# Optimization experiments

Measured on AMD Instinct MI355X. Metric: run time of the kernel, lower is better.

Reference implementation:

```python
import jax, jax.numpy as jnp
import numpy as np
from jax import lax


def _conv3x3(x, w, b):
    # x: [b,C,H,W], w: [Cout,Cin,3,3] (OIHW), same padding, stride 1
    y = lax.conv_general_dilated(
        x, w, window_strides=(1, 1), padding='SAME',
        dimension_numbers=('NCHW', 'OIHW', 'NCHW'))
    return y + b[None, :, None, None]


def setup_inputs() -> dict:
    key = jax.random.key(0)
    ks = jax.random.split(key, 8)
    b, C, H, W = 8, 256, 64, 64
    wscale = 0.02  # keep conv outputs O(1) so softmax logits are well-conditioned
    X = jax.random.normal(ks[0], (b, C, H, W), dtype=jnp.float32)
    w1 = jax.random.normal(ks[1], (C, C, 3, 3), dtype=jnp.float32) * wscale
    b1 = jax.random.normal(ks[2], (C,), dtype=jnp.float32) * 0.01
    w2 = jax.random.normal(ks[3], (C, C, 3, 3), dtype=jnp.float32) * wscale
    b2 = jax.random.normal(ks[4], (C,), dtype=jnp.float32) * 0.01
    w3 = jax.random.normal(ks[5], (C, C, 3, 3), dtype=jnp.float32) * wscale
    b3 = jax.random.normal(ks[6], (C,), dtype=jnp.float32) * 0.01
    # alpha_init=0 in the original makes the output identically zero; use a
    # small nonzero alpha so fwd/bwd are non-degenerate for correctness checks.
    alpha = jax.random.normal(ks[7], (), dtype=jnp.float32)
    return {"X": X, "w1": w1, "b1": b1, "w2": w2, "b2": b2,
            "w3": w3, "b3": b3, "alpha": alpha}


def reference(X, w1, b1, w2, b2, w3, b3, alpha):
    b, C, H, W = X.shape
    N = H * W
    A = _conv3x3(X, w1, b1).reshape(b, C, N)  # [b,C,N]
    B = _conv3x3(X, w2, b2).reshape(b, C, N)  # [b,C,N]
    D = _conv3x3(X, w3, b3).reshape(b, C, N)  # [b,C,N]
    # M = softmax(A^T B) over last dim; M: [b,N,N]
    M = jnp.einsum('bcn,bcm->bnm', A, B)
    M = jax.nn.softmax(M, axis=-1)
    # weighted_C = M @ D^T -> [b,N,C]; then to [b,C,H,W]
    out = jnp.einsum('bnm,bcm->bcn', M, D).reshape(b, C, H, W)
    return alpha * out
```

## Files before the change

### kernel.cpp

```cpp
#include <hip/hip_runtime.h>
#include <math.h>

#define BATCH 8
#define CCH   256
#define HH    64
#define WW    64
#define NN    4096

#define BNC   (BATCH * NN * CCH)
#define WELEMS (3 * 8 * 9 * 256 * 32)

typedef __bf16   bf16x8 __attribute__((ext_vector_type(8)));
typedef _Float16 f16x8  __attribute__((ext_vector_type(8)));
typedef _Float16 f16x4  __attribute__((ext_vector_type(4)));
typedef float    f32x4  __attribute__((ext_vector_type(4)));

__global__ void wtrans_kernel(const float* __restrict__ w1,
                              const float* __restrict__ w2,
                              const float* __restrict__ w3,
                              _Float16* __restrict__ Whi,
                              _Float16* __restrict__ Wlo) {
    int e = blockIdx.x * 256 + threadIdx.x;
    int t = e;
    const int ci  = t & 31;  t >>= 5;
    const int co  = t & 255; t >>= 8;
    const int tap = t % 9;   t /= 9;
    const int cc  = t & 7;   t >>= 3;
    const int conv = t;
    const float* src = (conv == 0) ? w1 : (conv == 1) ? w2 : w3;
    const float v = src[co * 2304 + (cc * 32 + ci) * 9 + tap];
    const _Float16 h = (_Float16)v;
    Whi[e] = h;
    Wlo[e] = (_Float16)(v - (float)h);
}

__global__ __launch_bounds__(256)
void xsplit_kernel(const float* __restrict__ X,
                   _Float16* __restrict__ Xhi, _Float16* __restrict__ Xlo) {
    __shared__ float T[64][65];
    const int h = blockIdx.x, c0 = blockIdx.y * 64, bb = blockIdx.z;
    const int t = threadIdx.x;
    const int row = t >> 2, q = (t & 3) * 16;
#pragma unroll
    for (int k = 0; k < 4; ++k) {
        float4 v = *(const float4*)&X[(((size_t)bb * CCH + c0 + row) * HH + h) * WW + q + k * 4];
        *(float4*)&T[row][q + k * 4] = v;
    }
    __syncthreads();
    f16x8 h0, h1, l0, l1;
#pragma unroll
    for (int j = 0; j < 8; ++j) {
        float v = T[q + j][row];
        _Float16 hh = (_Float16)v;
        h0[j] = hh; l0[j] = (_Float16)(v - (float)hh);
    }
#pragma unroll
    for (int j = 0; j < 8; ++j) {
        float v = T[q + 8 + j][row];
        _Float16 hh = (_Float16)v;
        h1[j] = hh; l1[j] = (_Float16)(v - (float)hh);
    }
    const size_t g = (((size_t)bb * HH + h) * WW + row) * CCH + c0 + q;
    *(f16x8*)(Xhi + g) = h0;  *(f16x8*)(Xhi + g + 8) = h1;
    *(f16x8*)(Xlo + g) = l0;  *(f16x8*)(Xlo + g + 8) = l1;
}

__global__ __launch_bounds__(512, 2)
void conv_mfma_kernel(const _Float16* __restrict__ Xhi, const _Float16* __restrict__ Xlo,
                      const _Float16* __restrict__ Whi, const _Float16* __restrict__ Wlo,
                      const float* __restrict__ b1, const float* __restrict__ b2,
                      const float* __restrict__ b3,
                      __bf16* __restrict__ Qhi, __bf16* __restrict__ Qlo,
                      __bf16* __restrict__ Khi, __bf16* __restrict__ Klo,
                      float* __restrict__ Dws) {
    const int h0   = blockIdx.x * 2;
    const int bb   = blockIdx.y;
    const int conv = blockIdx.z;
    const int tid  = threadIdx.x;
    const int wave = tid >> 6;
    const int lane = tid & 63;
    const int quad = lane >> 4;
    const int l16  = lane & 15;
    const int mg   = wave >> 2;
    const int ng   = wave & 3;

    __shared__ _Float16 XsH[4 * 66 * 32];
    __shared__ _Float16 XsL[4 * 66 * 32];

    const bool threePass = (conv < 2);
    const float* bias = (conv == 0) ? b1 : (conv == 1) ? b2 : b3;

    f32x4 acc[4][4];
#pragma unroll
    for (int j = 0; j < 4; ++j) {
        const float bv = bias[ng * 64 + j * 16 + l16];
#pragma unroll
        for (int i = 0; i < 4; ++i) acc[i][j] = (f32x4){bv, bv, bv, bv};
    }

    const f16x8 zf = {0, 0, 0, 0, 0, 0, 0, 0};
    const int xrow = tid >> 7;
    const int xw   = (tid >> 1) & 63;
    const int xch  = (tid & 1) * 16;
    const int xc0  = (tid & 1) * 2;

    if (tid < 256) {
        const int zr = tid >> 6, zc = ((tid >> 5) & 1) ? 65 : 0, zch = tid & 31;
        XsH[(zr * 66 + zc) * 32 + zch] = (_Float16)0;
        XsL[(zr * 66 + zc) * 32 + zch] = (_Float16)0;
    }

    int xb[3];
#pragma unroll
    for (int dw = 0; dw < 3; ++dw)
        xb[dw] = mg * 2112 + (l16 + dw) * 32 + ((quad ^ ((l16 + dw) & 3)) * 8);

    const int wloff = (ng * 64 + l16) * 32 + quad * 8;
    const _Float16* WhB = Whi + (size_t)conv * 589824;
    const _Float16* WlB = Wlo + (size_t)conv * 589824;

    f16x8 wbh[2][4], wbl[2][4];
#pragma unroll
    for (int j = 0; j < 4; ++j) {
        wbh[0][j] = *(const f16x8*)(WhB + wloff + j * 512);
        wbl[0][j] = zf;
        if (threePass) wbl[0][j] = *(const f16x8*)(WlB + wloff + j * 512);
    }

    for (int cc2 = 0; cc2 < 4; ++cc2) {
#pragma unroll
        for (int ccp = 0; ccp < 2; ++ccp) {
            const int cc = cc2 * 2 + ccp;
            __syncthreads();
            {
                const int h = h0 - 1 + xrow;
                f16x8 a0 = zf, a1 = zf, b0 = zf, b1v = zf;
                if ((unsigned)h < (unsigned)HH) {
                    const size_t g = (((size_t)bb * HH + h) * WW + xw) * CCH + cc * 32 + xch;
                    a0 = *(const f16x8*)(Xhi + g);  a1 = *(const f16x8*)(Xhi + g + 8);
                    if (threePass) { b0 = *(const f16x8*)(Xlo + g);  b1v = *(const f16x8*)(Xlo + g + 8); }
                }
                const int col = xw + 1;
                const int lbase = (xrow * 66 + col) * 32;
                const int s3 = col & 3;
                *(f16x8*)&XsH[lbase + ((xc0 ^ s3) * 8)]       = a0;
                *(f16x8*)&XsH[lbase + (((xc0 + 1) ^ s3) * 8)] = a1;
                if (threePass) {
                    *(f16x8*)&XsL[lbase + ((xc0 ^ s3) * 8)]       = b0;
                    *(f16x8*)&XsL[lbase + (((xc0 + 1) ^ s3) * 8)] = b1v;
                }
            }
            __syncthreads();

#pragma unroll
            for (int tap = 0; tap < 9; ++tap) {
                const int p  = (ccp + tap) & 1;
                const int np = p ^ 1;
                {
                    const int nst = cc * 9 + tap + 1;
                    const size_t nb = (size_t)(nst == 72 ? 0 : nst) * 8192 + wloff;
#pragma unroll
                    for (int j = 0; j < 4; ++j) {
                        wbh[np][j] = *(const f16x8*)(WhB + nb + j * 512);
                        if (threePass) wbl[np][j] = *(const f16x8*)(WlB + nb + j * 512);
                    }
                }
                const int dh = tap / 3, dw = tap % 3;
                f16x8 ah[4], al[4];
#pragma unroll
                for (int i = 0; i < 4; ++i) {
                    const int off = xb[dw] + dh * 2112 + i * 512;
                    ah[i] = *(const f16x8*)&XsH[off];
                    if (threePass) al[i] = *(const f16x8*)&XsL[off];
                }
#pragma unroll
                for (int j = 0; j < 4; ++j) {
                    if (threePass) {
#pragma unroll
                        for (int i = 0; i < 4; ++i) {
                            acc[i][j] = __builtin_amdgcn_mfma_f32_16x16x32_f16(ah[i], wbh[p][j], acc[i][j], 0, 0, 0);
                            acc[i][j] = __builtin_amdgcn_mfma_f32_16x16x32_f16(al[i], wbh[p][j], acc[i][j], 0, 0, 0);
                            acc[i][j] = __builtin_amdgcn_mfma_f32_16x16x32_f16(ah[i], wbl[p][j], acc[i][j], 0, 0, 0);
                        }
                    } else {
#pragma unroll
                        for (int i = 0; i < 4; ++i)
                            acc[i][j] = __builtin_amdgcn_mfma_f32_16x16x32_f16(ah[i], wbh[p][j], acc[i][j], 0, 0, 0);
                    }
                }
            }
        }
    }

    const size_t nb = (size_t)bb * NN + (size_t)(h0 + mg) * 64;
    if (threePass) {
        __bf16* Hi = conv ? Khi : Qhi;
        __bf16* Lo = conv ? Klo : Qlo;
#pragma unroll
        for (int i = 0; i < 4; ++i) {
            const int wx0 = i * 16 + quad * 4;
#pragma unroll
            for (int j = 0; j < 4; ++j) {
                const int co = ng * 64 + j * 16 + l16;
#pragma unroll
                for (int r = 0; r < 4; ++r) {
                    const float v = acc[i][j][r];
                    const size_t idx = (nb + wx0 + r) * CCH + co;
                    const __bf16 hq = (__bf16)v;
                    Hi[idx] = hq;
                    Lo[idx] = (__bf16)(v - (float)hq);
                }
            }
        }
    } else {
#pragma unroll
        for (int i = 0; i < 4; ++i) {
            const int wx0 = i * 16 + quad * 4;
#pragma unroll
            for (int j = 0; j < 4; ++j) {
                const int co = ng * 64 + j * 16 + l16;
#pragma unroll
                for (int r = 0; r < 4; ++r)
                    Dws[(nb + wx0 + r) * CCH + co] = acc[i][j][r];
            }
        }
    }
}

__global__ __launch_bounds__(256)
void transpose_v_kernel(const float* __restrict__ D, _Float16* __restrict__ Vt) {
    __shared__ float T[64][65];
    const int n0 = blockIdx.x * 64, c0 = blockIdx.y * 64, bb = blockIdx.z;
    const int t = threadIdx.x;
    const int row = t >> 2, q = (t & 3) * 16;
#pragma unroll
    for (int k = 0; k < 4; ++k) {
        float4 v = *(const float4*)(D + ((size_t)bb * NN + n0 + row) * CCH + c0 + q + k * 4);
        *(float4*)&T[row][q + k * 4] = v;
    }
    __syncthreads();
    f16x8 o0, o1;
#pragma unroll
    for (int j = 0; j < 8; ++j) o0[j] = (_Float16)T[q + j][row];
#pragma unroll
    for (int j = 0; j < 8; ++j) o1[j] = (_Float16)T[q + 8 + j][row];
    _Float16* dst = Vt + ((size_t)bb * CCH + c0 + row) * NN + n0 + q;
    *(f16x8*)dst = o0;
    *(f16x8*)(dst + 8) = o1;
}

__global__ __launch_bounds__(512, 2)
void attn_mfma_kernel(const __bf16* __restrict__ Qhi, const __bf16* __restrict__ Qlo,
                      const __bf16* __restrict__ Khi, const __bf16* __restrict__ Klo,
                      const _Float16* __restrict__ Vt, const float* __restrict__ alpha_p,
                      float* __restrict__ out) {
    const int bb = blockIdx.x & 7;
    const int qb = blockIdx.x >> 3;
    const int n0 = qb * 128;
    const int tid  = threadIdx.x;
    const int wave = tid >> 6;
    const int lane = tid & 63;
    const int quad = lane >> 4;
    const int l16  = lane & 15;
    const int xq   = l16 & 7;

    extern __shared__ __align__(16) unsigned char smem[];
    _Float16* PwA  = (_Float16*)(smem + 65536);
    float*    Ssc  = (float*)(smem + 100352);
    float*    Linv = (float*)(smem + 100864);
    _Float16* Pw   = PwA + wave * (16 * 136);

    bf16x8 qh[8], ql[8];
    {
        const size_t base = ((size_t)bb * NN + n0 + wave * 16 + l16) * CCH + quad * 8;
#pragma unroll
        for (int ks = 0; ks < 8; ++ks) {
            qh[ks] = *(const bf16x8*)(Qhi + base + ks * 32);
            ql[ks] = *(const bf16x8*)(Qlo + base + ks * 32);
        }
    }

    f32x4 Oacc[2][8];
#pragma unroll
    for (int cf = 0; cf < 2; ++cf)
#pragma unroll
        for (int qt = 0; qt < 8; ++qt) Oacc[cf][qt] = (f32x4){0.f, 0.f, 0.f, 0.f};
    float m_i = -INFINITY, l_i = 0.f;

    const int krow = tid >> 2, kq4 = tid & 3;

    bf16x8 kph[2], kpl[2];

    auto kload = [&](int m0_, int cc_) {
#pragma unroll
        for (int i = 0; i < 2; ++i) {
            const int u = kq4 * 2 + i;
            const size_t g = ((size_t)bb * NN + m0_ + krow) * CCH + cc_ * 64 + u * 8;
            kph[i] = *(const bf16x8*)(Khi + g);
            kpl[i] = *(const bf16x8*)(Klo + g);
        }
    };
    auto kwrite = [&](__bf16* H, __bf16* L) {
#pragma unroll
        for (int i = 0; i < 2; ++i) {
            const int u = kq4 * 2 + i;
            const int lo = krow * 64 + ((u ^ (krow & 7)) * 8);
            *(bf16x8*)&H[lo] = kph[i];
            *(bf16x8*)&L[lo] = kpl[i];
        }
    };

    f32x4 Sacc[8];
    auto schunk = [&](int cc, const __bf16* KH, const __bf16* KL) {
#pragma unroll
        for (int ks = 0; ks < 2; ++ks) {
            const int kq = cc * 2 + ks;
#pragma unroll
            for (int kvt = 0; kvt < 8; ++kvt) {
                const int off = (kvt * 16 + l16) * 64 + (((ks * 4 + quad) ^ xq) * 8);
                const bf16x8 kh = *(const bf16x8*)&KH[off];
                const bf16x8 kl = *(const bf16x8*)&KL[off];
                Sacc[kvt] = __builtin_amdgcn_mfma_f32_16x16x32_bf16(kh, qh[kq], Sacc[kvt], 0, 0, 0);
                Sacc[kvt] = __builtin_amdgcn_mfma_f32_16x16x32_bf16(kl, qh[kq], Sacc[kvt], 0, 0, 0);
                Sacc[kvt] = __builtin_amdgcn_mfma_f32_16x16x32_bf16(kh, ql[kq], Sacc[kvt], 0, 0, 0);
            }
        }
    };

    kload(0, 0);
    kwrite((__bf16*)smem, (__bf16*)(smem + 16384));
    __syncthreads();

    for (int t = 0; t < 32; ++t) {
        const int m0 = t * 128;
#pragma unroll
        for (int kvt = 0; kvt < 8; ++kvt) Sacc[kvt] = (f32x4){0.f, 0.f, 0.f, 0.f};

#pragma unroll
        for (int cc = 0; cc < 4; ++cc) {
            const int p = cc & 1;
            const __bf16* KH = (const __bf16*)(smem + p * 32768);
            const __bf16* KL = (const __bf16*)(smem + p * 32768 + 16384);
            __bf16* WH = (__bf16*)(smem + (p ^ 1) * 32768);
            __bf16* WL = (__bf16*)(smem + (p ^ 1) * 32768 + 16384);
            kload(cc < 3 ? m0 : ((t == 31) ? 0 : m0 + 128), (cc + 1) & 3);
            schunk(cc, KH, KL);
            kwrite(WH, WL);
            __syncthreads();
        }

        f16x8 vf[2][4];
#pragma unroll
        for (int cf = 0; cf < 2; ++cf)
#pragma unroll
            for (int kvf = 0; kvf < 4; ++kvf)
                vf[cf][kvf] = *(const f16x8*)(Vt +
                    ((size_t)bb * CCH + wave * 32 + cf * 16 + l16) * NN +
                    m0 + kvf * 32 + quad * 8);

        float mx = -INFINITY;
#pragma unroll
        for (int kvt = 0; kvt < 8; ++kvt)
#pragma unroll
            for (int r = 0; r < 4; ++r) mx = fmaxf(mx, Sacc[kvt][r]);
        mx = fmaxf(mx, __shfl_xor(mx, 16, 64));
        mx = fmaxf(mx, __shfl_xor(mx, 32, 64));
        const float mnew = fmaxf(m_i, mx);
        float rs = 0.f;
#pragma unroll
        for (int kvt = 0; kvt < 8; ++kvt) {
            f16x4 pw;
#pragma unroll
            for (int r = 0; r < 4; ++r) {
                const float p = __expf(Sacc[kvt][r] - mnew);
                rs += p;
                pw[r] = (_Float16)p;
            }
            *(f16x4*)&Pw[l16 * 136 + kvt * 16 + quad * 4] = pw;
        }
        rs += __shfl_xor(rs, 16, 64);
        rs += __shfl_xor(rs, 32, 64);
        const float scale = __expf(m_i - mnew);
        if (quad == 0) Ssc[wave * 16 + l16] = scale;
        l_i = l_i * scale + rs;
        m_i = mnew;
        __syncthreads();

        float sc[8];
#pragma unroll
        for (int qt = 0; qt < 8; ++qt) sc[qt] = Ssc[qt * 16 + l16];
#pragma unroll
        for (int cf = 0; cf < 2; ++cf)
#pragma unroll
            for (int qt = 0; qt < 8; ++qt) {
                Oacc[cf][qt][0] *= sc[qt];
                Oacc[cf][qt][1] *= sc[qt];
                Oacc[cf][qt][2] *= sc[qt];
                Oacc[cf][qt][3] *= sc[qt];
            }

#pragma unroll
        for (int qt = 0; qt < 8; ++qt) {
            const _Float16* Pq = PwA + qt * (16 * 136);
            f16x8 pf[4];
#pragma unroll
            for (int kvf = 0; kvf < 4; ++kvf)
                pf[kvf] = *(const f16x8*)&Pq[l16 * 136 + kvf * 32 + quad * 8];
#pragma unroll
            for (int cf = 0; cf < 2; ++cf)
#pragma unroll
                for (int kvf = 0; kvf < 4; ++kvf)
                    Oacc[cf][qt] = __builtin_amdgcn_mfma_f32_16x16x32_f16(vf[cf][kvf], pf[kvf], Oacc[cf][qt], 0, 0, 0);
        }
        __syncthreads();
    }

    const float alpha = *alpha_p;
    if (quad == 0) Linv[wave * 16 + l16] = alpha / l_i;
    __syncthreads();
#pragma unroll
    for (int qt = 0; qt < 8; ++qt) {
        const float inv = Linv[qt * 16 + l16];
#pragma unroll
        for (int cf = 0; cf < 2; ++cf)
#pragma unroll
            for (int r = 0; r < 4; ++r) {
                const int c = wave * 32 + cf * 16 + quad * 4 + r;
                out[((size_t)bb * CCH + c) * NN + n0 + qt * 16 + l16] = Oacc[cf][qt][r] * inv;
            }
    }
}

extern "C" void kernel_launch(void* const* d_in, const int* in_sizes, int n_in,
                              void* d_out, int out_size, void* d_ws, size_t ws_size,
                              hipStream_t stream) {
    const float* X  = (const float*)d_in[0];
    const float* w1 = (const float*)d_in[1];
    const float* b1 = (const float*)d_in[2];
    const float* w2 = (const float*)d_in[3];
    const float* b2 = (const float*)d_in[4];
    const float* w3 = (const float*)d_in[5];
    const float* b3 = (const float*)d_in[6];
    const float* alpha = (const float*)d_in[7];
    float* out = (float*)d_out;

    float*    Dws = (float*)d_ws;
    __bf16*   Qhi = (__bf16*)(Dws + (size_t)BNC);
    __bf16*   Qlo = Qhi + (size_t)BNC;
    __bf16*   Khi = Qlo + (size_t)BNC;
    __bf16*   Klo = Khi + (size_t)BNC;
    _Float16* Vt  = (_Float16*)(Klo + (size_t)BNC);
    _Float16* Xhi = Vt + (size_t)BNC;
    _Float16* Xlo = Xhi + (size_t)BNC;
    _Float16* Whi = Xlo + (size_t)BNC;
    _Float16* Wlo = Whi + (size_t)WELEMS;

    wtrans_kernel<<<dim3(WELEMS / 256), 256, 0, stream>>>(w1, w2, w3, Whi, Wlo);

    xsplit_kernel<<<dim3(HH, CCH / 64, BATCH), 256, 0, stream>>>(X, Xhi, Xlo);

    conv_mfma_kernel<<<dim3(HH / 2, BATCH, 3), 512, 0, stream>>>(
        Xhi, Xlo, Whi, Wlo, b1, b2, b3, Qhi, Qlo, Khi, Klo, Dws);

    transpose_v_kernel<<<dim3(NN / 64, CCH / 64, BATCH), 256, 0, stream>>>(Dws, Vt);

    attn_mfma_kernel<<<dim3(256), 512, 101376, stream>>>(
        Qhi, Qlo, Khi, Klo, Vt, alpha, out);
}
```

Baseline: 591.8 us.

## Halve attention query tile to 64 rows with 4 waves and single-buffered K

The attention kernel now uses 64 query rows per block with 256 threads (4 waves) and twice as many blocks. Each wave covers 64 output channels instead of 32. K staging in shared memory drops from double to single buffering, which adds an extra barrier per chunk. V fragments are loaded per channel group inside the PV loop instead of before the softmax. The intent is to halve shared memory per block and raise parallelism and occupancy, at the cost of more redundant K/V traffic per query row and less overlap between K loads and MFMA work.

```diff
diff --git a/kernel.cpp b/kernel.cpp
--- a/kernel.cpp
+++ b/kernel.cpp
@@ -249,14 +249,14 @@
     *(f16x8*)(dst + 8) = o1;
 }
 
-__global__ __launch_bounds__(512, 2)
+__global__ __launch_bounds__(256, 2)
 void attn_mfma_kernel(const __bf16* __restrict__ Qhi, const __bf16* __restrict__ Qlo,
                       const __bf16* __restrict__ Khi, const __bf16* __restrict__ Klo,
                       const _Float16* __restrict__ Vt, const float* __restrict__ alpha_p,
                       float* __restrict__ out) {
     const int bb = blockIdx.x & 7;
     const int qb = blockIdx.x >> 3;
-    const int n0 = qb * 128;
+    const int n0 = qb * 64;
     const int tid  = threadIdx.x;
     const int wave = tid >> 6;
     const int lane = tid & 63;
@@ -265,9 +265,11 @@
     const int xq   = l16 & 7;
 
     extern __shared__ __align__(16) unsigned char smem[];
-    _Float16* PwA  = (_Float16*)(smem + 65536);
-    float*    Ssc  = (float*)(smem + 100352);
-    float*    Linv = (float*)(smem + 100864);
+    __bf16*   KsHi = (__bf16*)(smem);
+    __bf16*   KsLo = (__bf16*)(smem + 16384);
+    _Float16* PwA  = (_Float16*)(smem + 32768);
+    float*    Ssc  = (float*)(smem + 50176);
+    float*    Linv = (float*)(smem + 50432);
     _Float16* Pw   = PwA + wave * (16 * 136);
 
     bf16x8 qh[8], ql[8];
@@ -280,46 +282,46 @@
         }
     }
 
-    f32x4 Oacc[2][8];
-#pragma unroll
-    for (int cf = 0; cf < 2; ++cf)
-#pragma unroll
-        for (int qt = 0; qt < 8; ++qt) Oacc[cf][qt] = (f32x4){0.f, 0.f, 0.f, 0.f};
+    f32x4 Oacc[4][4];
+#pragma unroll
+    for (int cf = 0; cf < 4; ++cf)
+#pragma unroll
+        for (int qt = 0; qt < 4; ++qt) Oacc[cf][qt] = (f32x4){0.f, 0.f, 0.f, 0.f};
     float m_i = -INFINITY, l_i = 0.f;
 
-    const int krow = tid >> 2, kq4 = tid & 3;
-
-    bf16x8 kph[2], kpl[2];
+    const int krow = tid >> 1, kh2 = tid & 1;
+
+    bf16x8 kph[4], kpl[4];
 
     auto kload = [&](int m0_, int cc_) {
 #pragma unroll
-        for (int i = 0; i < 2; ++i) {
-            const int u = kq4 * 2 + i;
+        for (int i = 0; i < 4; ++i) {
+            const int u = kh2 * 4 + i;
             const size_t g = ((size_t)bb * NN + m0_ + krow) * CCH + cc_ * 64 + u * 8;
             kph[i] = *(const bf16x8*)(Khi + g);
             kpl[i] = *(const bf16x8*)(Klo + g);
         }
     };
-    auto kwrite = [&](__bf16* H, __bf16* L) {
-#pragma unroll
-        for (int i = 0; i < 2; ++i) {
-            const int u = kq4 * 2 + i;
+    auto kwrite = [&]() {
+#pragma unroll
+        for (int i = 0; i < 4; ++i) {
+            const int u = kh2 * 4 + i;
             const int lo = krow * 64 + ((u ^ (krow & 7)) * 8);
-            *(bf16x8*)&H[lo] = kph[i];
-            *(bf16x8*)&L[lo] = kpl[i];
+            *(bf16x8*)&KsHi[lo] = kph[i];
+            *(bf16x8*)&KsLo[lo] = kpl[i];
         }
     };
 
     f32x4 Sacc[8];
-    auto schunk = [&](int cc, const __bf16* KH, const __bf16* KL) {
+    auto schunk = [&](int cc) {
 #pragma unroll
         for (int ks = 0; ks < 2; ++ks) {
             const int kq = cc * 2 + ks;
 #pragma unroll
             for (int kvt = 0; kvt < 8; ++kvt) {
                 const int off = (kvt * 16 + l16) * 64 + (((ks * 4 + quad) ^ xq) * 8);
-                const bf16x8 kh = *(const bf16x8*)&KH[off];
-                const bf16x8 kl = *(const bf16x8*)&KL[off];
+                const bf16x8 kh = *(const bf16x8*)&KsHi[off];
+                const bf16x8 kl = *(const bf16x8*)&KsLo[off];
                 Sacc[kvt] = __builtin_amdgcn_mfma_f32_16x16x32_bf16(kh, qh[kq], Sacc[kvt], 0, 0, 0);
                 Sacc[kvt] = __builtin_amdgcn_mfma_f32_16x16x32_bf16(kl, qh[kq], Sacc[kvt], 0, 0, 0);
                 Sacc[kvt] = __builtin_amdgcn_mfma_f32_16x16x32_bf16(kh, ql[kq], Sacc[kvt], 0, 0, 0);
@@ -328,7 +330,7 @@
     };
 
     kload(0, 0);
-    kwrite((__bf16*)smem, (__bf16*)(smem + 16384));
+    kwrite();
     __syncthreads();
 
     for (int t = 0; t < 32; ++t) {
@@ -338,25 +340,12 @@
 
 #pragma unroll
         for (int cc = 0; cc < 4; ++cc) {
-            const int p = cc & 1;
-            const __bf16* KH = (const __bf16*)(smem + p * 32768);
-            const __bf16* KL = (const __bf16*)(smem + p * 32768 + 16384);
-            __bf16* WH = (__bf16*)(smem + (p ^ 1) * 32768);
-            __bf16* WL = (__bf16*)(smem + (p ^ 1) * 32768 + 16384);
             kload(cc < 3 ? m0 : ((t == 31) ? 0 : m0 + 128), (cc + 1) & 3);
-            schunk(cc, KH, KL);
-            kwrite(WH, WL);
+            schunk(cc);
             __syncthreads();
-        }
-
-        f16x8 vf[2][4];
-#pragma unroll
-        for (int cf = 0; cf < 2; ++cf)
-#pragma unroll
-            for (int kvf = 0; kvf < 4; ++kvf)
-                vf[cf][kvf] = *(const f16x8*)(Vt +
-                    ((size_t)bb * CCH + wave * 32 + cf * 16 + l16) * NN +
-                    m0 + kvf * 32 + quad * 8);
+            kwrite();
+            __syncthreads();
+        }
 
         float mx = -INFINITY;
 #pragma unroll
@@ -386,31 +375,38 @@
         m_i = mnew;
         __syncthreads();
 
-        float sc[8];
-#pragma unroll
-        for (int qt = 0; qt < 8; ++qt) sc[qt] = Ssc[qt * 16 + l16];
-#pragma unroll
-        for (int cf = 0; cf < 2; ++cf)
-#pragma unroll
-            for (int qt = 0; qt < 8; ++qt) {
+        float sc[4];
+#pragma unroll
+        for (int qt = 0; qt < 4; ++qt) sc[qt] = Ssc[qt * 16 + l16];
+#pragma unroll
+        for (int cf = 0; cf < 4; ++cf)
+#pragma unroll
+            for (int qt = 0; qt < 4; ++qt) {
                 Oacc[cf][qt][0] *= sc[qt];
                 Oacc[cf][qt][1] *= sc[qt];
                 Oacc[cf][qt][2] *= sc[qt];
                 Oacc[cf][qt][3] *= sc[qt];
             }
 
-#pragma unroll
-        for (int qt = 0; qt < 8; ++qt) {
-            const _Float16* Pq = PwA + qt * (16 * 136);
-            f16x8 pf[4];
+        f16x8 pf[4][4];
+#pragma unroll
+        for (int qt = 0; qt < 4; ++qt)
 #pragma unroll
             for (int kvf = 0; kvf < 4; ++kvf)
-                pf[kvf] = *(const f16x8*)&Pq[l16 * 136 + kvf * 32 + quad * 8];
-#pragma unroll
-            for (int cf = 0; cf < 2; ++cf)
+                pf[qt][kvf] = *(const f16x8*)&PwA[qt * 2176 + l16 * 136 + kvf * 32 + quad * 8];
+#pragma unroll
+        for (int cf = 0; cf < 4; ++cf) {
+            f16x8 vfc[4];
+#pragma unroll
+            for (int kvf = 0; kvf < 4; ++kvf)
+                vfc[kvf] = *(const f16x8*)(Vt +
+                    ((size_t)bb * CCH + wave * 64 + cf * 16 + l16) * NN +
+                    m0 + kvf * 32 + quad * 8);
+#pragma unroll
+            for (int qt = 0; qt < 4; ++qt)
 #pragma unroll
                 for (int kvf = 0; kvf < 4; ++kvf)
-                    Oacc[cf][qt] = __builtin_amdgcn_mfma_f32_16x16x32_f16(vf[cf][kvf], pf[kvf], Oacc[cf][qt], 0, 0, 0);
+                    Oacc[cf][qt] = __builtin_amdgcn_mfma_f32_16x16x32_f16(vfc[kvf], pf[qt][kvf], Oacc[cf][qt], 0, 0, 0);
         }
         __syncthreads();
     }
@@ -419,13 +415,13 @@
     if (quad == 0) Linv[wave * 16 + l16] = alpha / l_i;
     __syncthreads();
 #pragma unroll
-    for (int qt = 0; qt < 8; ++qt) {
+    for (int qt = 0; qt < 4; ++qt) {
         const float inv = Linv[qt * 16 + l16];
 #pragma unroll
-        for (int cf = 0; cf < 2; ++cf)
+        for (int cf = 0; cf < 4; ++cf)
 #pragma unroll
             for (int r = 0; r < 4; ++r) {
-                const int c = wave * 32 + cf * 16 + quad * 4 + r;
+                const int c = wave * 64 + cf * 16 + quad * 4 + r;
                 out[((size_t)bb * CCH + c) * NN + n0 + qt * 16 + l16] = Oacc[cf][qt][r] * inv;
             }
     }
@@ -464,6 +460,6 @@
 
     transpose_v_kernel<<<dim3(NN / 64, CCH / 64, BATCH), 256, 0, stream>>>(Dws, Vt);
 
-    attn_mfma_kernel<<<dim3(256), 512, 101376, stream>>>(
+    attn_mfma_kernel<<<dim3(512), 256, 50688, stream>>>(
         Qhi, Qlo, Khi, Klo, Vt, alpha, out);
 }
```

After: 626.8 us. +5.9%, slower.

## Triple-buffer K tiles in LDS and prefetch next tile during PV phase

Applied to the files above, without the earlier changes.

Replaces the double-buffered K chunk pipeline with a three-slot rotating LDS buffer. The per-tile barriers in the QK^T loop drop from four to two, and the next tile's first two K chunks are loaded and written during the P·V MFMA phase. The aim is to hide global K loads behind the PV compute and cut synchronisation. The cost is LDS use rising from about 99KB to 131KB per block, which may limit occupancy under launch_bounds(512,2), and a more intricate buffer-rotation schedule.

```diff
diff --git a/kernel.cpp b/kernel.cpp
--- a/kernel.cpp
+++ b/kernel.cpp
@@ -265,9 +265,9 @@
     const int xq   = l16 & 7;
 
     extern __shared__ __align__(16) unsigned char smem[];
-    _Float16* PwA  = (_Float16*)(smem + 65536);
-    float*    Ssc  = (float*)(smem + 100352);
-    float*    Linv = (float*)(smem + 100864);
+    _Float16* PwA  = (_Float16*)(smem + 98304);
+    float*    Ssc  = (float*)(smem + 133120);
+    float*    Linv = (float*)(smem + 133632);
     _Float16* Pw   = PwA + wave * (16 * 136);
 
     bf16x8 qh[8], ql[8];
@@ -300,7 +300,9 @@
             kpl[i] = *(const bf16x8*)(Klo + g);
         }
     };
-    auto kwrite = [&](__bf16* H, __bf16* L) {
+    auto kwrite = [&](unsigned char* base) {
+        __bf16* H = (__bf16*)base;
+        __bf16* L = (__bf16*)(base + 16384);
 #pragma unroll
         for (int i = 0; i < 2; ++i) {
             const int u = kq4 * 2 + i;
@@ -311,7 +313,9 @@
     };
 
     f32x4 Sacc[8];
-    auto schunk = [&](int cc, const __bf16* KH, const __bf16* KL) {
+    auto schunk = [&](int cc, const unsigned char* base) {
+        const __bf16* KH = (const __bf16*)base;
+        const __bf16* KL = (const __bf16*)(base + 16384);
 #pragma unroll
         for (int ks = 0; ks < 2; ++ks) {
             const int kq = cc * 2 + ks;
@@ -328,26 +332,33 @@
     };
 
     kload(0, 0);
-    kwrite((__bf16*)smem, (__bf16*)(smem + 16384));
+    kwrite(smem);
+    kload(0, 1);
+    kwrite(smem + 32768);
     __syncthreads();
+
+    int rot = 0;
 
     for (int t = 0; t < 32; ++t) {
         const int m0 = t * 128;
+        const int m0n = (t == 31) ? 0 : m0 + 128;
+        unsigned char* P0 = smem + rot * 32768;
+        unsigned char* P1 = smem + ((rot + 1) % 3) * 32768;
+        unsigned char* F  = smem + ((rot + 2) % 3) * 32768;
+
 #pragma unroll
         for (int kvt = 0; kvt < 8; ++kvt) Sacc[kvt] = (f32x4){0.f, 0.f, 0.f, 0.f};
 
-#pragma unroll
-        for (int cc = 0; cc < 4; ++cc) {
-            const int p = cc & 1;
-            const __bf16* KH = (const __bf16*)(smem + p * 32768);
-            const __bf16* KL = (const __bf16*)(smem + p * 32768 + 16384);
-            __bf16* WH = (__bf16*)(smem + (p ^ 1) * 32768);
-            __bf16* WL = (__bf16*)(smem + (p ^ 1) * 32768 + 16384);
-            kload(cc < 3 ? m0 : ((t == 31) ? 0 : m0 + 128), (cc + 1) & 3);
-            schunk(cc, KH, KL);
-            kwrite(WH, WL);
-            __syncthreads();
-        }
+        kload(m0, 2);
+        schunk(0, P0);
+        kwrite(F);
+        kload(m0, 3);
+        schunk(1, P1);
+        __syncthreads();
+        kwrite(P0);
+        schunk(2, F);
+        __syncthreads();
+        schunk(3, P0);
 
         f16x8 vf[2][4];
 #pragma unroll
@@ -399,8 +410,9 @@
                 Oacc[cf][qt][3] *= sc[qt];
             }
 
-#pragma unroll
-        for (int qt = 0; qt < 8; ++qt) {
+        kload(m0n, 0);
+#pragma unroll
+        for (int qt = 0; qt < 4; ++qt) {
             const _Float16* Pq = PwA + qt * (16 * 136);
             f16x8 pf[4];
 #pragma unroll
@@ -412,7 +424,25 @@
                 for (int kvf = 0; kvf < 4; ++kvf)
                     Oacc[cf][qt] = __builtin_amdgcn_mfma_f32_16x16x32_f16(vf[cf][kvf], pf[kvf], Oacc[cf][qt], 0, 0, 0);
         }
+        kwrite(P1);
+        kload(m0n, 1);
+#pragma unroll
+        for (int qt = 4; qt < 8; ++qt) {
+            const _Float16* Pq = PwA + qt * (16 * 136);
+            f16x8 pf[4];
+#pragma unroll
+            for (int kvf = 0; kvf < 4; ++kvf)
+                pf[kvf] = *(const f16x8*)&Pq[l16 * 136 + kvf * 32 + quad * 8];
+#pragma unroll
+            for (int cf = 0; cf < 2; ++cf)
+#pragma unroll
+                for (int kvf = 0; kvf < 4; ++kvf)
+                    Oacc[cf][qt] = __builtin_amdgcn_mfma_f32_16x16x32_f16(vf[cf][kvf], pf[kvf], Oacc[cf][qt], 0, 0, 0);
+        }
+        kwrite(F);
         __syncthreads();
+
+        rot = (rot + 1) == 3 ? 0 : rot + 1;
     }
 
     const float alpha = *alpha_p;
@@ -464,6 +494,6 @@
 
     transpose_v_kernel<<<dim3(NN / 64, CCH / 64, BATCH), 256, 0, stream>>>(Dws, Vt);
 
-    attn_mfma_kernel<<<dim3(256), 512, 101376, stream>>>(
+    attn_mfma_kernel<<<dim3(256), 512, 134144, stream>>>(
         Qhi, Qlo, Khi, Klo, Vt, alpha, out);
 }
```

After: 559.6 us. 1.06x faster.
